# Kernel tuning notes

Hardware: AMD Instinct MI355X
Metric: run time of the kernel (lower is better)

Reference implementation:

```python
import jax, jax.numpy as jnp
import numpy as np

HEADS = 16
D_MODEL = 1024
HEAD_DIM = D_MODEL // HEADS
NEG = -1e15


def setup_inputs() -> dict:
    key = jax.random.key(0)
    ks = jax.random.split(key, 13)
    B, L = 2, 2048
    scale = 1.0 / np.sqrt(D_MODEL)
    inp = {
        'q': jax.random.normal(ks[0], (B, L, D_MODEL), jnp.float32),
        'k': jax.random.normal(ks[1], (B, L, D_MODEL), jnp.float32),
        'v': jax.random.normal(ks[2], (B, L, D_MODEL), jnp.float32),
        'mask': jax.random.randint(ks[3], (B, 1, 1, L), 0, 2, jnp.int32),
        'Wq': jax.random.normal(ks[4], (D_MODEL, D_MODEL), jnp.float32) * scale,
        'bq': jax.random.normal(ks[5], (D_MODEL,), jnp.float32) * scale,
        'Wk': jax.random.normal(ks[6], (D_MODEL, D_MODEL), jnp.float32) * scale,
        'bk': jax.random.normal(ks[7], (D_MODEL,), jnp.float32) * scale,
        'Wv': jax.random.normal(ks[8], (D_MODEL, D_MODEL), jnp.float32) * scale,
        'bv': jax.random.normal(ks[9], (D_MODEL,), jnp.float32) * scale,
        'Wo': jax.random.normal(ks[10], (D_MODEL, D_MODEL), jnp.float32) * scale,
        'bo': jax.random.normal(ks[11], (D_MODEL,), jnp.float32) * scale,
    }
    return inp


def _split_heads(x):
    B, L, _ = x.shape
    return x.reshape(B, L, HEADS, HEAD_DIM).transpose(0, 2, 1, 3)  # [B,H,L,Dh]


def reference(q, k, v, mask, Wq, bq, Wk, bk, Wv, bv, Wo, bo):
    B, L, _ = q.shape
    # torch Linear: y = x @ W.T + b
    qh = _split_heads(q @ Wq.T + bq)
    kh = _split_heads(k @ Wk.T + bk)
    vh = _split_heads(v @ Wv.T + bv)
    scores = jnp.einsum('bhqd,bhkd->bhqk', qh, kh) / jnp.sqrt(jnp.float32(HEAD_DIM))
    scores = scores + mask.astype(scores.dtype) * NEG
    weights = jax.nn.softmax(scores, axis=-1)
    attn = jnp.einsum('bhqk,bhkd->bhqd', weights, vh)  # [B,H,L,Dh]
    attn = attn.transpose(0, 2, 1, 3).reshape(B, L, D_MODEL)
    return attn @ Wo.T + bo
```

## Files before the change

### kernel.cpp

```cpp
#include <hip/hip_runtime.h>
#include <stdint.h>

typedef __bf16 bf16;
typedef __attribute__((ext_vector_type(8))) __bf16 bf16x8;
typedef __attribute__((ext_vector_type(4))) float f32x4;

#define SEQ   2048
#define DM    1024
#define NH    16
#define HD    64
#define MROWS 4096

__device__ __forceinline__ void glds16(const bf16* g, bf16* l) {
  __builtin_amdgcn_global_load_lds(
      (__attribute__((address_space(1))) unsigned int*)(g),
      (__attribute__((address_space(3))) unsigned int*)(l),
      16, 0, 0);
}

__global__ void conv3(const float* __restrict__ s0, const float* __restrict__ s1,
                      const float* __restrict__ s2, bf16* __restrict__ d0,
                      bf16* __restrict__ d1, bf16* __restrict__ d2) {
  const float* s = blockIdx.z == 0 ? s0 : (blockIdx.z == 1 ? s1 : s2);
  bf16* d = blockIdx.z == 0 ? d0 : (blockIdx.z == 1 ? d1 : d2);
  const size_t i = ((size_t)blockIdx.x * 256 + threadIdx.x) * 8;
  const f32x4 a = *(const f32x4*)(s + i);
  const f32x4 b = *(const f32x4*)(s + i + 4);
  bf16x8 r;
  r[0] = (bf16)a[0]; r[1] = (bf16)a[1]; r[2] = (bf16)a[2]; r[3] = (bf16)a[3];
  r[4] = (bf16)b[0]; r[5] = (bf16)b[1]; r[6] = (bf16)b[2]; r[7] = (bf16)b[3];
  *(bf16x8*)(d + i) = r;
}

__global__ void conv4(const float* __restrict__ s0, const float* __restrict__ s1,
                      const float* __restrict__ s2, const float* __restrict__ s3,
                      bf16* __restrict__ d0, bf16* __restrict__ d1,
                      bf16* __restrict__ d2, bf16* __restrict__ d3) {
  const float* s = blockIdx.z == 0 ? s0 : (blockIdx.z == 1 ? s1 : (blockIdx.z == 2 ? s2 : s3));
  bf16* d = blockIdx.z == 0 ? d0 : (blockIdx.z == 1 ? d1 : (blockIdx.z == 2 ? d2 : d3));
  const size_t i = ((size_t)blockIdx.x * 256 + threadIdx.x) * 8;
  const f32x4 a = *(const f32x4*)(s + i);
  const f32x4 b = *(const f32x4*)(s + i + 4);
  bf16x8 r;
  r[0] = (bf16)a[0]; r[1] = (bf16)a[1]; r[2] = (bf16)a[2]; r[3] = (bf16)a[3];
  r[4] = (bf16)b[0]; r[5] = (bf16)b[1]; r[6] = (bf16)b[2]; r[7] = (bf16)b[3];
  *(bf16x8*)(d + i) = r;
}

__global__ __launch_bounds__(256, 2) void proj_bf16(
    const bf16* __restrict__ A0, const bf16* __restrict__ A1,
    const bf16* __restrict__ W0, const bf16* __restrict__ W1,
    const float* __restrict__ Bb0, const float* __restrict__ Bb1,
    void* __restrict__ O0, void* __restrict__ O1, int mode)
{
  __shared__ __align__(16) bf16 sA[128 * 64];
  __shared__ __align__(16) bf16 sB[128 * 64];

  const int z = blockIdx.z;
  const bf16* A  = z ? A1 : A0;
  const bf16* Wp = z ? W1 : W0;
  const float* Bv = z ? Bb1 : Bb0;
  void* Out = z ? O1 : O0;

  const int tid  = threadIdx.x;
  const int lane = tid & 63;
  const int wv   = tid >> 6;
  const int quad = lane >> 4;
  const int colx = lane & 15;
  const int m0 = blockIdx.y * 128;
  const int n0 = blockIdx.x * 128;
  const int rm = (wv >> 1) * 64;
  const int rn = (wv & 1) * 64;

  f32x4 acc[4][4];
#pragma unroll
  for (int mi = 0; mi < 4; ++mi)
#pragma unroll
    for (int ni = 0; ni < 4; ++ni) {
      f32x4 zz = {0.f, 0.f, 0.f, 0.f};
      acc[mi][ni] = zz;
    }

  for (int kt = 0; kt < 16; ++kt) {
    const int k0 = kt * 64;
    __syncthreads();
#pragma unroll
    for (int i = 0; i < 4; ++i) {
      const int f = i * 256 + tid;
      const int row = f >> 3;
      const int c = f & 7;
      const int cc = c ^ (row & 7);
      glds16(A  + (size_t)(m0 + row) * DM + k0 + cc * 8, sA + f * 8);
      glds16(Wp + (size_t)(n0 + row) * DM + k0 + cc * 8, sB + f * 8);
    }
    __syncthreads();

    bf16x8 af[4][2], bfr[4][2];
#pragma unroll
    for (int t4 = 0; t4 < 4; ++t4) {
#pragma unroll
      for (int ks = 0; ks < 2; ++ks) {
        const int ra = rm + t4 * 16 + colx;
        af[t4][ks] = *(const bf16x8*)(sA + ra * 64 + (((ks * 4 + quad) ^ (ra & 7)) * 8));
        const int rb = rn + t4 * 16 + colx;
        bfr[t4][ks] = *(const bf16x8*)(sB + rb * 64 + (((ks * 4 + quad) ^ (rb & 7)) * 8));
      }
    }
#pragma unroll
    for (int mi = 0; mi < 4; ++mi)
#pragma unroll
      for (int ni = 0; ni < 4; ++ni) {
        acc[mi][ni] = __builtin_amdgcn_mfma_f32_16x16x32_bf16(af[mi][0], bfr[ni][0], acc[mi][ni], 0, 0, 0);
        acc[mi][ni] = __builtin_amdgcn_mfma_f32_16x16x32_bf16(af[mi][1], bfr[ni][1], acc[mi][ni], 0, 0, 0);
      }
  }

  if (mode == 2) {
#pragma unroll
    for (int mi = 0; mi < 4; ++mi) {
#pragma unroll
      for (int r = 0; r < 4; ++r) {
        const int m = m0 + rm + mi * 16 + quad * 4 + r;
        const float bias = Bv[m];
        const int hh = m >> 6, d = m & 63;
#pragma unroll
        for (int ni = 0; ni < 4; ++ni) {
          const int n = n0 + rn + ni * 16 + colx;
          const int b = n >> 11, l = n & 2047;
          const int lb = l >> 7, li = l & 127;
          const int perm = (li & 15) * 8 + ((li >> 4) & 7);
          const float v = acc[mi][ni][r] + bias;
          ((bf16*)Out)[(((size_t)(b * NH + hh) * HD + d) * SEQ) + lb * 128 + perm] = (bf16)v;
        }
      }
    }
  } else {
    const float scale = (mode == 0 && z == 0) ? 0.125f : 1.0f;
#pragma unroll
    for (int ni = 0; ni < 4; ++ni) {
      const int n = n0 + rn + ni * 16 + colx;
      const float bias = Bv[n];
#pragma unroll
      for (int mi = 0; mi < 4; ++mi) {
#pragma unroll
        for (int r = 0; r < 4; ++r) {
          const int m = m0 + rm + mi * 16 + quad * 4 + r;
          const float v = (acc[mi][ni][r] + bias) * scale;
          if (mode == 3) {
            ((float*)Out)[(size_t)m * DM + n] = v;
          } else {
            const int b = m >> 11, l = m & 2047, hh = n >> 6, d = n & 63;
            ((bf16*)Out)[((size_t)(b * NH + hh) * SEQ + l) * HD + d] = (bf16)v;
          }
        }
      }
    }
  }
}

__global__ __launch_bounds__(256, 2) void attn_kernel(
    const bf16* __restrict__ Qh, const bf16* __restrict__ Kh, const bf16* __restrict__ Vt,
    const int* __restrict__ mask, bf16* __restrict__ At)
{
  __shared__ __align__(16) bf16 sK[128 * 64];
  __shared__ __align__(16) bf16 sVt[80 * 128];
  __shared__ __align__(16) bf16 sP[4][32 * 128];

  const int tid  = threadIdx.x;
  const int lane = tid & 63;
  const int wv   = tid >> 6;
  const int quad = lane >> 4;
  const int colx = lane & 15;
  const int bh = blockIdx.y;
  const int b  = bh >> 4;
  const int h  = bh & 15;
  const int q0 = blockIdx.x * 128;
  const size_t base  = (size_t)bh * SEQ * HD;
  const size_t baseV = (size_t)bh * HD * SEQ;

  {
    const int row = 64 + (tid >> 4);
    const float val = (row == 64) ? 1.0f : 0.0f;
    bf16x8 vv;
#pragma unroll
    for (int j = 0; j < 8; ++j) vv[j] = (bf16)val;
    *(bf16x8*)(sVt + row * 128 + (tid & 15) * 8) = vv;
  }

  bf16x8 qf[2][2];
#pragma unroll
  for (int half = 0; half < 2; ++half) {
    const int qrow = q0 + wv * 32 + half * 16 + colx;
    qf[half][0] = *(const bf16x8*)(Qh + base + (size_t)qrow * HD + quad * 8);
    qf[half][1] = *(const bf16x8*)(Qh + base + (size_t)qrow * HD + 32 + quad * 8);
  }

  f32x4 o[2][5];
#pragma unroll
  for (int half = 0; half < 2; ++half)
#pragma unroll
    for (int dt = 0; dt < 5; ++dt) {
      f32x4 zz = {0.f, 0.f, 0.f, 0.f};
      o[half][dt] = zz;
    }
  bf16* sPw = &sP[wv][0];

  for (int kc = 0; kc < 16; ++kc) {
    const int key0 = kc * 128;
    __syncthreads();
#pragma unroll
    for (int i = 0; i < 4; ++i) {
      const int f = i * 256 + tid;
      const int kr = f >> 3;
      const int ck = (f & 7) ^ (kr & 7);
      glds16(Kh + base + (size_t)(key0 + kr) * HD + ck * 8, sK + f * 8);
      const int dr = f >> 4;
      const int cv = (f & 15) ^ (dr & 15);
      glds16(Vt + baseV + (size_t)dr * SEQ + key0 + cv * 8, sVt + f * 8);
    }
    float mreg[8];
#pragma unroll
    for (int nt = 0; nt < 8; ++nt)
      mreg[nt] = (mask[b * SEQ + key0 + nt * 16 + colx] ? -1e30f : 0.0f) - 16.0f;
    __syncthreads();

#pragma unroll
    for (int half = 0; half < 2; ++half) {
      f32x4 s8[8];
#pragma unroll
      for (int nt = 0; nt < 8; ++nt) {
        f32x4 s = {0.f, 0.f, 0.f, 0.f};
        const int krow = nt * 16 + colx;
#pragma unroll
        for (int ks = 0; ks < 2; ++ks) {
          const bf16x8 kf = *(const bf16x8*)(sK + krow * 64 + (((ks * 4 + quad) ^ (krow & 7)) * 8));
          s = __builtin_amdgcn_mfma_f32_16x16x32_bf16(qf[half][ks], kf, s, 0, 0, 0);
        }
        s8[nt] = s;
      }
#pragma unroll
      for (int r = 0; r < 4; ++r) {
        bf16x8 pk;
#pragma unroll
        for (int nt = 0; nt < 8; ++nt)
          pk[nt] = (bf16)__expf(s8[nt][r] + mreg[nt]);
        const int row = half * 16 + quad * 4 + r;
        *(bf16x8*)(sPw + row * 128 + ((colx ^ (row & 15)) * 8)) = pk;
      }
    }

#pragma unroll
    for (int ks = 0; ks < 4; ++ks) {
      const int ch = ((ks * 4 + quad) ^ colx) * 8;
      const bf16x8 pf0 = *(const bf16x8*)(sPw + colx * 128 + ch);
      const bf16x8 pf1 = *(const bf16x8*)(sPw + (16 + colx) * 128 + ch);
#pragma unroll
      for (int dt = 0; dt < 5; ++dt) {
        const int drow = (dt < 4) ? (dt * 16 + colx) : (64 + colx);
        const bf16x8 vf = *(const bf16x8*)(sVt + drow * 128 + ch);
        o[0][dt] = __builtin_amdgcn_mfma_f32_16x16x32_bf16(pf0, vf, o[0][dt], 0, 0, 0);
        o[1][dt] = __builtin_amdgcn_mfma_f32_16x16x32_bf16(pf1, vf, o[1][dt], 0, 0, 0);
      }
    }
  }

#pragma unroll
  for (int half = 0; half < 2; ++half) {
#pragma unroll
    for (int r = 0; r < 4; ++r) {
      const float lsum = __shfl(o[half][4][r], (lane & 48));
      const float inv = 1.0f / lsum;
      const int q = q0 + wv * 32 + half * 16 + quad * 4 + r;
#pragma unroll
      for (int dt = 0; dt < 4; ++dt) {
        At[((size_t)(b * SEQ + q)) * DM + h * HD + dt * 16 + colx] =
            (bf16)(o[half][dt][r] * inv);
      }
    }
  }
}

extern "C" void kernel_launch(void* const* d_in, const int* in_sizes, int n_in,
                              void* d_out, int out_size, void* d_ws, size_t ws_size,
                              hipStream_t stream) {
  (void)in_sizes; (void)n_in; (void)out_size; (void)ws_size;
  const float* q    = (const float*)d_in[0];
  const float* k    = (const float*)d_in[1];
  const float* v    = (const float*)d_in[2];
  const int*   mask = (const int*)d_in[3];
  const float* Wq   = (const float*)d_in[4];
  const float* bq   = (const float*)d_in[5];
  const float* Wk   = (const float*)d_in[6];
  const float* bk   = (const float*)d_in[7];
  const float* Wv   = (const float*)d_in[8];
  const float* bv   = (const float*)d_in[9];
  const float* Wo   = (const float*)d_in[10];
  const float* bo   = (const float*)d_in[11];
  float* out = (float*)d_out;

  const size_t T = (size_t)MROWS * DM;
  const size_t WT = (size_t)DM * DM;
  bf16* ws  = (bf16*)d_ws;
  bf16* qb  = ws;
  bf16* kb  = qb + T;
  bf16* vb  = kb + T;
  bf16* Wqb = vb + T;
  bf16* Wkb = Wqb + WT;
  bf16* Wvb = Wkb + WT;
  bf16* Wob = Wvb + WT;
  bf16* Qh  = Wob + WT;
  bf16* Kh  = Qh + T;
  bf16* Vt  = Kh + T;
  bf16* At  = Vt + T;

  dim3 blk(256);
  conv3<<<dim3(2048, 1, 3), blk, 0, stream>>>(q, k, v, qb, kb, vb);
  conv4<<<dim3(512, 1, 4), blk, 0, stream>>>(Wq, Wk, Wv, Wo, Wqb, Wkb, Wvb, Wob);
  proj_bf16<<<dim3(8, 32, 2), blk, 0, stream>>>(qb, kb, Wqb, Wkb, bq, bk, Qh, Kh, 0);
  proj_bf16<<<dim3(32, 8, 1), blk, 0, stream>>>(Wvb, nullptr, vb, nullptr, bv, nullptr, Vt, nullptr, 2);
  attn_kernel<<<dim3(16, 32), blk, 0, stream>>>(Qh, Kh, Vt, mask, At);
  proj_bf16<<<dim3(8, 32, 1), blk, 0, stream>>>(At, nullptr, Wob, nullptr, bo, nullptr, out, nullptr, 3);
}
```

Baseline: 236.9 us.

## Fuse activation fp32-to-bf16 conversion into QKV GEMM and double-buffer LDS

Drops the separate conversion kernel for q/k/v. The projection kernels now read fp32 activations directly and convert them to bf16 while staging into LDS. The Q, K and V projections are merged into one launch with three z-slices, and both the QKV and output GEMMs gain double-buffered LDS staging so the next tile's loads overlap the current tile's MFMA work. This removes a full fp32 read plus bf16 write-and-reread of the activations and one launch. In exchange, the register-path fp32 loads are synchronous, LDS use doubles, and the fp32 A tile must be read at twice the bytes.

Measured after the change: 282.1 us. +19.1%, slower.

```diff
diff --git a/kernel.cpp b/kernel.cpp
--- a/kernel.cpp
+++ b/kernel.cpp
@@ -18,18 +18,13 @@
       16, 0, 0);
 }
 
-__global__ void conv3(const float* __restrict__ s0, const float* __restrict__ s1,
-                      const float* __restrict__ s2, bf16* __restrict__ d0,
-                      bf16* __restrict__ d1, bf16* __restrict__ d2) {
-  const float* s = blockIdx.z == 0 ? s0 : (blockIdx.z == 1 ? s1 : s2);
-  bf16* d = blockIdx.z == 0 ? d0 : (blockIdx.z == 1 ? d1 : d2);
-  const size_t i = ((size_t)blockIdx.x * 256 + threadIdx.x) * 8;
-  const f32x4 a = *(const f32x4*)(s + i);
-  const f32x4 b = *(const f32x4*)(s + i + 4);
+static __device__ __forceinline__ bf16x8 cvt_f32x8(const float* __restrict__ p) {
+  const f32x4 a = *(const f32x4*)p;
+  const f32x4 b = *(const f32x4*)(p + 4);
   bf16x8 r;
   r[0] = (bf16)a[0]; r[1] = (bf16)a[1]; r[2] = (bf16)a[2]; r[3] = (bf16)a[3];
   r[4] = (bf16)b[0]; r[5] = (bf16)b[1]; r[6] = (bf16)b[2]; r[7] = (bf16)b[3];
-  *(bf16x8*)(d + i) = r;
+  return r;
 }
 
 __global__ void conv4(const float* __restrict__ s0, const float* __restrict__ s1,
@@ -39,28 +34,141 @@
   const float* s = blockIdx.z == 0 ? s0 : (blockIdx.z == 1 ? s1 : (blockIdx.z == 2 ? s2 : s3));
   bf16* d = blockIdx.z == 0 ? d0 : (blockIdx.z == 1 ? d1 : (blockIdx.z == 2 ? d2 : d3));
   const size_t i = ((size_t)blockIdx.x * 256 + threadIdx.x) * 8;
-  const f32x4 a = *(const f32x4*)(s + i);
-  const f32x4 b = *(const f32x4*)(s + i + 4);
-  bf16x8 r;
-  r[0] = (bf16)a[0]; r[1] = (bf16)a[1]; r[2] = (bf16)a[2]; r[3] = (bf16)a[3];
-  r[4] = (bf16)b[0]; r[5] = (bf16)b[1]; r[6] = (bf16)b[2]; r[7] = (bf16)b[3];
-  *(bf16x8*)(d + i) = r;
-}
-
-__global__ __launch_bounds__(256, 2) void proj_bf16(
-    const bf16* __restrict__ A0, const bf16* __restrict__ A1,
-    const bf16* __restrict__ W0, const bf16* __restrict__ W1,
-    const float* __restrict__ Bb0, const float* __restrict__ Bb1,
-    void* __restrict__ O0, void* __restrict__ O1, int mode)
+  *(bf16x8*)(d + i) = cvt_f32x8(s + i);
+}
+
+__global__ __launch_bounds__(256, 2) void proj_qkv(
+    const float* __restrict__ qf, const float* __restrict__ kf, const float* __restrict__ vf,
+    const bf16* __restrict__ Wqb, const bf16* __restrict__ Wkb, const bf16* __restrict__ Wvb,
+    const float* __restrict__ bq, const float* __restrict__ bk, const float* __restrict__ bv,
+    bf16* __restrict__ Qh, bf16* __restrict__ Kh, bf16* __restrict__ Vt)
 {
-  __shared__ __align__(16) bf16 sA[128 * 64];
-  __shared__ __align__(16) bf16 sB[128 * 64];
+  __shared__ __align__(16) bf16 sA[2][128 * 64];
+  __shared__ __align__(16) bf16 sB[2][128 * 64];
 
   const int z = blockIdx.z;
-  const bf16* A  = z ? A1 : A0;
-  const bf16* Wp = z ? W1 : W0;
-  const float* Bv = z ? Bb1 : Bb0;
-  void* Out = z ? O1 : O0;
+  const float* Af = (z == 0) ? qf : kf;
+  const bf16*  Ab = Wvb;
+  const bf16*  Bb = (z == 0) ? Wqb : Wkb;
+  const float* Bf = vf;
+  const float* Bv = (z == 0) ? bq : ((z == 1) ? bk : bv);
+  const bool a_f32 = (z < 2);
+
+  const int tid  = threadIdx.x;
+  const int lane = tid & 63;
+  const int wv   = tid >> 6;
+  const int quad = lane >> 4;
+  const int colx = lane & 15;
+  const int m0 = (z == 2) ? (int)blockIdx.x * 128 : (int)blockIdx.y * 128;
+  const int n0 = (z == 2) ? (int)blockIdx.y * 128 : (int)blockIdx.x * 128;
+  const int rm = (wv >> 1) * 64;
+  const int rn = (wv & 1) * 64;
+
+  int srow[4], schunk[4];
+#pragma unroll
+  for (int i = 0; i < 4; ++i) {
+    const int f = i * 256 + tid;
+    srow[i] = f >> 3;
+    schunk[i] = (f & 7) ^ (srow[i] & 7);
+  }
+
+  f32x4 acc[4][4];
+#pragma unroll
+  for (int mi = 0; mi < 4; ++mi)
+#pragma unroll
+    for (int ni = 0; ni < 4; ++ni) {
+      f32x4 zz = {0.f, 0.f, 0.f, 0.f};
+      acc[mi][ni] = zz;
+    }
+
+  auto stage = [&](int kt, int bu) {
+    const int k0 = kt * 64;
+#pragma unroll
+    for (int i = 0; i < 4; ++i) {
+      const int f = i * 256 + tid;
+      const int row = srow[i], cc = schunk[i];
+      if (a_f32) {
+        *(bf16x8*)(&sA[bu][f * 8]) = cvt_f32x8(Af + (size_t)(m0 + row) * DM + k0 + cc * 8);
+        glds16(Bb + (size_t)(n0 + row) * DM + k0 + cc * 8, &sB[bu][f * 8]);
+      } else {
+        glds16(Ab + (size_t)(m0 + row) * DM + k0 + cc * 8, &sA[bu][f * 8]);
+        *(bf16x8*)(&sB[bu][f * 8]) = cvt_f32x8(Bf + (size_t)(n0 + row) * DM + k0 + cc * 8);
+      }
+    }
+  };
+
+  stage(0, 0);
+  for (int kt = 0; kt < 16; ++kt) {
+    const int bu = kt & 1;
+    __syncthreads();
+    if (kt < 15) stage(kt + 1, bu ^ 1);
+
+    bf16x8 af[4][2], bfr[4][2];
+#pragma unroll
+    for (int t4 = 0; t4 < 4; ++t4) {
+#pragma unroll
+      for (int ks = 0; ks < 2; ++ks) {
+        const int ra = rm + t4 * 16 + colx;
+        af[t4][ks] = *(const bf16x8*)(&sA[bu][ra * 64 + (((ks * 4 + quad) ^ (ra & 7)) * 8)]);
+        const int rb = rn + t4 * 16 + colx;
+        bfr[t4][ks] = *(const bf16x8*)(&sB[bu][rb * 64 + (((ks * 4 + quad) ^ (rb & 7)) * 8)]);
+      }
+    }
+#pragma unroll
+    for (int mi = 0; mi < 4; ++mi)
+#pragma unroll
+      for (int ni = 0; ni < 4; ++ni) {
+        acc[mi][ni] = __builtin_amdgcn_mfma_f32_16x16x32_bf16(af[mi][0], bfr[ni][0], acc[mi][ni], 0, 0, 0);
+        acc[mi][ni] = __builtin_amdgcn_mfma_f32_16x16x32_bf16(af[mi][1], bfr[ni][1], acc[mi][ni], 0, 0, 0);
+      }
+  }
+
+  if (z == 2) {
+#pragma unroll
+    for (int mi = 0; mi < 4; ++mi) {
+#pragma unroll
+      for (int r = 0; r < 4; ++r) {
+        const int m = m0 + rm + mi * 16 + quad * 4 + r;
+        const float bias = Bv[m];
+        const int hh = m >> 6, d = m & 63;
+#pragma unroll
+        for (int ni = 0; ni < 4; ++ni) {
+          const int n = n0 + rn + ni * 16 + colx;
+          const int b = n >> 11, l = n & 2047;
+          const int lb = l >> 7, li = l & 127;
+          const int perm = (li & 15) * 8 + ((li >> 4) & 7);
+          Vt[(((size_t)(b * NH + hh) * HD + d) * SEQ) + lb * 128 + perm] =
+              (bf16)(acc[mi][ni][r] + bias);
+        }
+      }
+    }
+  } else {
+    bf16* Out = (z == 0) ? Qh : Kh;
+    const float scale = (z == 0) ? 0.125f : 1.0f;
+#pragma unroll
+    for (int ni = 0; ni < 4; ++ni) {
+      const int n = n0 + rn + ni * 16 + colx;
+      const float bias = Bv[n];
+#pragma unroll
+      for (int mi = 0; mi < 4; ++mi) {
+#pragma unroll
+        for (int r = 0; r < 4; ++r) {
+          const int m = m0 + rm + mi * 16 + quad * 4 + r;
+          const float v = (acc[mi][ni][r] + bias) * scale;
+          const int b = m >> 11, l = m & 2047, hh = n >> 6, d = n & 63;
+          Out[((size_t)(b * NH + hh) * SEQ + l) * HD + d] = (bf16)v;
+        }
+      }
+    }
+  }
+}
+
+__global__ __launch_bounds__(256, 2) void proj_out(
+    const bf16* __restrict__ At, const bf16* __restrict__ Wob,
+    const float* __restrict__ bo, float* __restrict__ Out)
+{
+  __shared__ __align__(16) bf16 sA[2][128 * 64];
+  __shared__ __align__(16) bf16 sB[2][128 * 64];
 
   const int tid  = threadIdx.x;
   const int lane = tid & 63;
@@ -81,19 +189,23 @@
       acc[mi][ni] = zz;
     }
 
-  for (int kt = 0; kt < 16; ++kt) {
+  auto stage = [&](int kt, int bu) {
     const int k0 = kt * 64;
-    __syncthreads();
 #pragma unroll
     for (int i = 0; i < 4; ++i) {
       const int f = i * 256 + tid;
       const int row = f >> 3;
-      const int c = f & 7;
-      const int cc = c ^ (row & 7);
-      glds16(A  + (size_t)(m0 + row) * DM + k0 + cc * 8, sA + f * 8);
-      glds16(Wp + (size_t)(n0 + row) * DM + k0 + cc * 8, sB + f * 8);
-    }
+      const int cc = (f & 7) ^ (row & 7);
+      glds16(At  + (size_t)(m0 + row) * DM + k0 + cc * 8, &sA[bu][f * 8]);
+      glds16(Wob + (size_t)(n0 + row) * DM + k0 + cc * 8, &sB[bu][f * 8]);
+    }
+  };
+
+  stage(0, 0);
+  for (int kt = 0; kt < 16; ++kt) {
+    const int bu = kt & 1;
     __syncthreads();
+    if (kt < 15) stage(kt + 1, bu ^ 1);
 
     bf16x8 af[4][2], bfr[4][2];
 #pragma unroll
@@ -101,9 +213,9 @@
 #pragma unroll
       for (int ks = 0; ks < 2; ++ks) {
         const int ra = rm + t4 * 16 + colx;
-        af[t4][ks] = *(const bf16x8*)(sA + ra * 64 + (((ks * 4 + quad) ^ (ra & 7)) * 8));
+        af[t4][ks] = *(const bf16x8*)(&sA[bu][ra * 64 + (((ks * 4 + quad) ^ (ra & 7)) * 8)]);
         const int rb = rn + t4 * 16 + colx;
-        bfr[t4][ks] = *(const bf16x8*)(sB + rb * 64 + (((ks * 4 + quad) ^ (rb & 7)) * 8));
+        bfr[t4][ks] = *(const bf16x8*)(&sB[bu][rb * 64 + (((ks * 4 + quad) ^ (rb & 7)) * 8)]);
       }
     }
 #pragma unroll
@@ -115,44 +227,16 @@
       }
   }
 
-  if (mode == 2) {
+#pragma unroll
+  for (int ni = 0; ni < 4; ++ni) {
+    const int n = n0 + rn + ni * 16 + colx;
+    const float bias = bo[n];
 #pragma unroll
     for (int mi = 0; mi < 4; ++mi) {
 #pragma unroll
       for (int r = 0; r < 4; ++r) {
         const int m = m0 + rm + mi * 16 + quad * 4 + r;
-        const float bias = Bv[m];
-        const int hh = m >> 6, d = m & 63;
-#pragma unroll
-        for (int ni = 0; ni < 4; ++ni) {
-          const int n = n0 + rn + ni * 16 + colx;
-          const int b = n >> 11, l = n & 2047;
-          const int lb = l >> 7, li = l & 127;
-          const int perm = (li & 15) * 8 + ((li >> 4) & 7);
-          const float v = acc[mi][ni][r] + bias;
-          ((bf16*)Out)[(((size_t)(b * NH + hh) * HD + d) * SEQ) + lb * 128 + perm] = (bf16)v;
-        }
-      }
-    }
-  } else {
-    const float scale = (mode == 0 && z == 0) ? 0.125f : 1.0f;
-#pragma unroll
-    for (int ni = 0; ni < 4; ++ni) {
-      const int n = n0 + rn + ni * 16 + colx;
-      const float bias = Bv[n];
-#pragma unroll
-      for (int mi = 0; mi < 4; ++mi) {
-#pragma unroll
-        for (int r = 0; r < 4; ++r) {
-          const int m = m0 + rm + mi * 16 + quad * 4 + r;
-          const float v = (acc[mi][ni][r] + bias) * scale;
-          if (mode == 3) {
-            ((float*)Out)[(size_t)m * DM + n] = v;
-          } else {
-            const int b = m >> 11, l = m & 2047, hh = n >> 6, d = n & 63;
-            ((bf16*)Out)[((size_t)(b * NH + hh) * SEQ + l) * HD + d] = (bf16)v;
-          }
-        }
+        Out[(size_t)m * DM + n] = acc[mi][ni][r] + bias;
       }
     }
   }
@@ -301,10 +385,7 @@
   const size_t T = (size_t)MROWS * DM;
   const size_t WT = (size_t)DM * DM;
   bf16* ws  = (bf16*)d_ws;
-  bf16* qb  = ws;
-  bf16* kb  = qb + T;
-  bf16* vb  = kb + T;
-  bf16* Wqb = vb + T;
+  bf16* Wqb = ws;
   bf16* Wkb = Wqb + WT;
   bf16* Wvb = Wkb + WT;
   bf16* Wob = Wvb + WT;
@@ -314,10 +395,9 @@
   bf16* At  = Vt + T;
 
   dim3 blk(256);
-  conv3<<<dim3(2048, 1, 3), blk, 0, stream>>>(q, k, v, qb, kb, vb);
   conv4<<<dim3(512, 1, 4), blk, 0, stream>>>(Wq, Wk, Wv, Wo, Wqb, Wkb, Wvb, Wob);
-  proj_bf16<<<dim3(8, 32, 2), blk, 0, stream>>>(qb, kb, Wqb, Wkb, bq, bk, Qh, Kh, 0);
-  proj_bf16<<<dim3(32, 8, 1), blk, 0, stream>>>(Wvb, nullptr, vb, nullptr, bv, nullptr, Vt, nullptr, 2);
+  proj_qkv<<<dim3(8, 32, 3), blk, 0, stream>>>(q, k, v, Wqb, Wkb, Wvb, bq, bk, bv,
+                                               Qh, Kh, Vt);
   attn_kernel<<<dim3(16, 32), blk, 0, stream>>>(Qh, Kh, Vt, mask, At);
-  proj_bf16<<<dim3(8, 32, 1), blk, 0, stream>>>(At, nullptr, Wob, nullptr, bo, nullptr, out, nullptr, 3);
-}
+  proj_out<<<dim3(8, 32), blk, 0, stream>>>(At, Wob, bo, out);
+}
```
